# Kernel optimization log

Measured on AMD Instinct MI355X. Metric: run time of the kernel, lower is better.

The kernel has to match this reference:

```python
import jax, jax.numpy as jnp
import numpy as np

B, S, E, H, D = 384, 128, 512, 4, 128  # batch, seq(block), embed, heads, head_dim


def setup_inputs() -> dict:
    key = jax.random.key(0)
    ks = jax.random.split(key, 6)
    scale = 1.0 / np.sqrt(E)  # lecun_normal-ish fan-in scaling
    return {
        "x": jax.random.normal(ks[0], (B, S, E), dtype=jnp.float32),
        "Wq": jax.random.normal(ks[1], (E, E), dtype=jnp.float32) * scale,
        "bq": jnp.zeros((E,), dtype=jnp.float32),
        "Wk": jax.random.normal(ks[2], (E, E), dtype=jnp.float32) * scale,
        "bk": jnp.zeros((E,), dtype=jnp.float32),
        "Wv": jax.random.normal(ks[3], (E, E), dtype=jnp.float32) * scale,
        "bv": jnp.zeros((E,), dtype=jnp.float32),
        "Wo": jax.random.normal(ks[4], (E, E), dtype=jnp.float32) * scale,
        "bo": jnp.zeros((E,), dtype=jnp.float32),
    }


def reference(x, Wq, bq, Wk, bk, Wv, bv, Wo, bo):
    # Projections, then split heads: [B,S,E] -> [B,S,H,D]
    q = (x @ Wq + bq).reshape(B, S, H, D)
    k = (x @ Wk + bk).reshape(B, S, H, D)
    v = (x @ Wv + bv).reshape(B, S, H, D)
    # NOTE: original applies no 1/sqrt(D) scaling and no mask.
    scores = jnp.einsum("BSHD,BTHD->BHST", q, k)  # [B,H,S,T]
    weights = jax.nn.softmax(scores, axis=-1)
    out = jnp.einsum("BHST,BTHD->BSHD", weights, v).reshape(B, S, E)
    return out @ Wo + bo
```

## Files before the change

### kernel.cpp

```cpp
#include <hip/hip_runtime.h>
#include <hip/hip_bf16.h>
#include <cstdint>


#define EMB 512

typedef __attribute__((ext_vector_type(4))) float    f32x4;
typedef __attribute__((ext_vector_type(8))) _Float16 f16x8;

#define MFMA16(a, b, c) __builtin_amdgcn_mfma_f32_16x16x32_f16((a), (b), (c), 0, 0, 0)

__device__ __forceinline__ int swz128(int row, int col) {
    return row * 128 + (col ^ (((row >> 2) & 3) << 4));
}
__device__ __forceinline__ int swz64(int row, int col) {
    return row * 64 + (col ^ (((row >> 2) & 3) << 4));
}

__device__ __forceinline__ void gld_lds16(const _Float16* g, _Float16* l) {
    __builtin_amdgcn_global_load_lds(
        (const __attribute__((address_space(1))) void*)g,
        (__attribute__((address_space(3))) void*)l, 16, 0, 0);
}

__device__ __forceinline__ void stage64(_Float16* lds, const _Float16* gbase,
                                        int grow0, int k0, int wave, int lane) {
#pragma unroll
    for (int i = 0; i < 4; ++i) {
        int idx = wave * 256 + i * 64 + lane;
        int n   = idx >> 3;
        int kb  = (idx & 7) ^ (((n >> 2) & 3) << 1);
        gld_lds16(gbase + (grow0 + n) * EMB + k0 + kb * 8,
                  lds + wave * 2048 + i * 512);
    }
}

#define ZACC(A)                                   \
    _Pragma("unroll") for (int _i = 0; _i < 2; ++_i) \
    _Pragma("unroll") for (int _j = 0; _j < 8; ++_j) \
        A[_i][_j] = (f32x4){0.f, 0.f, 0.f, 0.f};

__global__ void k_prep(const float* __restrict__ x, _Float16* __restrict__ xh,
                       const float* __restrict__ Wq, const float* __restrict__ Wk,
                       const float* __restrict__ Wv, const float* __restrict__ Wo,
                       _Float16* __restrict__ Wqkvt, _Float16* __restrict__ Wot) {
    __shared__ float t[32][33];
    const int g = blockIdx.x, tid = threadIdx.x;
    if (g < 12288) {
        long i = ((long)g * 256 + tid) * 8;
        f32x4 a = *(const f32x4*)(x + i);
        f32x4 b = *(const f32x4*)(x + i + 4);
        f16x8 o;
        o[0] = (_Float16)a[0]; o[1] = (_Float16)a[1];
        o[2] = (_Float16)a[2]; o[3] = (_Float16)a[3];
        o[4] = (_Float16)b[0]; o[5] = (_Float16)b[1];
        o[6] = (_Float16)b[2]; o[7] = (_Float16)b[3];
        *(f16x8*)(xh + i) = o;
        return;
    }
    const int tb = g - 12288;
    const int z = tb >> 8, t2 = tb & 255;
    const float* W = (z == 0) ? Wq : (z == 1) ? Wk : (z == 2) ? Wv : Wo;
    _Float16* Wt = (z < 3) ? (Wqkvt + (long)z * 512 * EMB) : Wot;
    const int tx = tid & 31, ty = tid >> 5;
    const int k0 = (t2 & 15) * 32, n0 = (t2 >> 4) * 32;
#pragma unroll
    for (int i = 0; i < 4; ++i)
        t[ty + i * 8][tx] = W[(k0 + ty + i * 8) * EMB + n0 + tx];
    __syncthreads();
#pragma unroll
    for (int i = 0; i < 4; ++i)
        Wt[(n0 + ty + i * 8) * EMB + k0 + tx] = (_Float16)t[tx][ty + i * 8];
}

__global__ __launch_bounds__(256, 4)
void k_qkv(const _Float16* __restrict__ xh, const _Float16* __restrict__ Wqkvt,
           const float* __restrict__ bq, const float* __restrict__ bk,
           const float* __restrict__ bv,
           _Float16* __restrict__ qb, _Float16* __restrict__ kb,
           _Float16* __restrict__ vtb) {
    __shared__ _Float16 S[2][128 * 64];
    _Float16* SA = S[0];
    _Float16* SB = S[1];
    const int tid = threadIdx.x, wave = tid >> 6, lane = tid & 63;
    const int l15 = lane & 15, quad = lane >> 4;
    const int g = blockIdx.x;
    const int xcd = g & 7, r = g >> 3;
    const int bb = xcd * 48 + r / 12, j = r % 12;
    const int m0 = bb * 128;
    const bool vswap = (j >= 8);
    const _Float16* As = vswap ? SB : SA;
    const _Float16* Bs = vswap ? SA : SB;
    f32x4 acc[2][8];
    ZACC(acc);
    for (int k0 = 0; k0 < EMB; k0 += 64) {
        stage64(SA, xh, m0, k0, wave, lane);
        stage64(SB, Wqkvt, j * 128, k0, wave, lane);
        __syncthreads();
#pragma unroll
        for (int ktl = 0; ktl < 2; ++ktl) {
            int cb = ktl * 32 + quad * 8;
            f16x8 a0 = *(const f16x8*)&As[swz64(wave * 32 + l15, cb)];
            f16x8 a1 = *(const f16x8*)&As[swz64(wave * 32 + 16 + l15, cb)];
#pragma unroll
            for (int nt = 0; nt < 8; ++nt) {
                f16x8 bbf = *(const f16x8*)&Bs[swz64(nt * 16 + l15, cb)];
                acc[0][nt] = MFMA16(a0, bbf, acc[0][nt]);
                acc[1][nt] = MFMA16(a1, bbf, acc[1][nt]);
            }
        }
        __syncthreads();
    }
    _Float16* SC = &S[0][0];
    if (!vswap) {
        const float* bias = (j < 4) ? bq : bk;
        const int nc0 = (j & 3) * 128;
#pragma unroll
        for (int nt = 0; nt < 8; ++nt) {
            int col = nt * 16 + l15;
            float bz = bias[nc0 + col];
#pragma unroll
            for (int mt = 0; mt < 2; ++mt)
#pragma unroll
                for (int rr = 0; rr < 4; ++rr) {
                    int row = wave * 32 + mt * 16 + quad * 4 + rr;
                    SC[swz128(row, col)] = (_Float16)(acc[mt][nt][rr] + bz);
                }
        }
        __syncthreads();
        _Float16* dst = (j < 4) ? qb : kb;
#pragma unroll
        for (int i = 0; i < 8; ++i) {
            int idx = i * 256 + tid;
            int row = idx >> 4, col = (idx & 15) * 8;
            f16x8 v = *(const f16x8*)&SC[row * 128 + (col ^ (((row >> 2) & 3) << 4))];
            *(f16x8*)(dst + (long)(m0 + row) * EMB + nc0 + col) = v;
        }
    } else {
        const int hv = j - 8;
#pragma unroll
        for (int mt = 0; mt < 2; ++mt)
#pragma unroll
            for (int rr = 0; rr < 4; ++rr) {
                int row = wave * 32 + mt * 16 + quad * 4 + rr;
                float bz = bv[hv * 128 + row];
#pragma unroll
                for (int nt = 0; nt < 8; ++nt) {
                    int col = nt * 16 + l15;
                    SC[swz128(row, col)] = (_Float16)(acc[mt][nt][rr] + bz);
                }
            }
        __syncthreads();
        _Float16* dst = vtb + (long)(bb * 4 + hv) * 128 * 128;
#pragma unroll
        for (int i = 0; i < 8; ++i) {
            int idx = i * 256 + tid;
            int row = idx >> 4, col = (idx & 15) * 8;
            f16x8 v = *(const f16x8*)&SC[row * 128 + (col ^ (((row >> 2) & 3) << 4))];
            *(f16x8*)(dst + row * 128 + col) = v;
        }
    }
}

__global__ __launch_bounds__(256, 4)
void k_core(const _Float16* __restrict__ qb, const _Float16* __restrict__ kb,
            const _Float16* __restrict__ vtb, _Float16* __restrict__ attn) {
    __shared__ _Float16 SP[128 * 128];
    const int tid = threadIdx.x, wave = tid >> 6, lane = tid & 63;
    const int l15 = lane & 15, quad = lane >> 4;
    const int g = blockIdx.x;
    const int xcd = g & 7, r = g >> 3;
    const int b = xcd * 48 + (r >> 2), h = r & 3;
    const int sRow0 = b * 128, wRow0 = h * 128;
    const _Float16* vt = vtb + (long)(b * 4 + h) * 128 * 128;
    f32x4 acc[2][8];

    ZACC(acc);
#pragma unroll
    for (int kt = 0; kt < 4; ++kt) {
        int ca = kt * 32 + quad * 8;
        const _Float16* qrow = qb + (long)(sRow0 + wave * 32 + l15) * EMB + wRow0 + ca;
        f16x8 q0 = *(const f16x8*)qrow;
        f16x8 q1 = *(const f16x8*)(qrow + 16 * EMB);
#pragma unroll
        for (int nt = 0; nt < 8; ++nt) {
            f16x8 kf = *(const f16x8*)(kb + (long)(sRow0 + nt * 16 + l15) * EMB + wRow0 + ca);
            acc[0][nt] = MFMA16(q0, kf, acc[0][nt]);
            acc[1][nt] = MFMA16(q1, kf, acc[1][nt]);
        }
    }
#pragma unroll
    for (int mt = 0; mt < 2; ++mt)
#pragma unroll
        for (int rr = 0; rr < 4; ++rr) {
            float mx = acc[mt][0][rr];
#pragma unroll
            for (int nt = 1; nt < 8; ++nt) mx = fmaxf(mx, acc[mt][nt][rr]);
            mx = fmaxf(mx, __shfl_xor(mx, 1));
            mx = fmaxf(mx, __shfl_xor(mx, 2));
            mx = fmaxf(mx, __shfl_xor(mx, 4));
            mx = fmaxf(mx, __shfl_xor(mx, 8));
            float sm = 0.f;
#pragma unroll
            for (int nt = 0; nt < 8; ++nt) {
                float e = __expf(acc[mt][nt][rr] - mx);
                acc[mt][nt][rr] = e;
                sm += e;
            }
            sm += __shfl_xor(sm, 1);
            sm += __shfl_xor(sm, 2);
            sm += __shfl_xor(sm, 4);
            sm += __shfl_xor(sm, 8);
            float inv = 1.0f / sm;
#pragma unroll
            for (int nt = 0; nt < 8; ++nt) acc[mt][nt][rr] *= inv;
        }

#pragma unroll
    for (int mt = 0; mt < 2; ++mt)
#pragma unroll
        for (int nt = 0; nt < 8; ++nt) {
            int col = nt * 16 + l15;
#pragma unroll
            for (int rr = 0; rr < 4; ++rr) {
                int row = wave * 32 + mt * 16 + quad * 4 + rr;
                SP[swz128(row, col)] = (_Float16)acc[mt][nt][rr];
            }
        }
    __syncthreads();

    ZACC(acc);
#pragma unroll
    for (int kt = 0; kt < 4; ++kt) {
        int ca = kt * 32 + quad * 8;
        int rp = wave * 32 + l15;
        f16x8 p0 = *(const f16x8*)&SP[swz128(rp, ca)];
        f16x8 p1 = *(const f16x8*)&SP[swz128(rp + 16, ca)];
#pragma unroll
        for (int nt = 0; nt < 8; ++nt) {
            f16x8 vf = *(const f16x8*)(vt + (nt * 16 + l15) * 128 + ca);
            acc[0][nt] = MFMA16(p0, vf, acc[0][nt]);
            acc[1][nt] = MFMA16(p1, vf, acc[1][nt]);
        }
    }
    __syncthreads();

#pragma unroll
    for (int mt = 0; mt < 2; ++mt)
#pragma unroll
        for (int nt = 0; nt < 8; ++nt) {
            int col = nt * 16 + l15;
#pragma unroll
            for (int rr = 0; rr < 4; ++rr) {
                int row = wave * 32 + mt * 16 + quad * 4 + rr;
                SP[swz128(row, col)] = (_Float16)acc[mt][nt][rr];
            }
        }
    __syncthreads();
#pragma unroll
    for (int i = 0; i < 8; ++i) {
        int idx = i * 256 + tid;
        int row = idx >> 4, col = (idx & 15) * 8;
        f16x8 v = *(const f16x8*)&SP[row * 128 + (col ^ (((row >> 2) & 3) << 4))];
        *(f16x8*)(attn + (long)(sRow0 + row) * EMB + wRow0 + col) = v;
    }
}

__global__ __launch_bounds__(256, 4)
void k_out(const _Float16* __restrict__ attn, const _Float16* __restrict__ Wot,
           const float* __restrict__ bo, float* __restrict__ out) {
    __shared__ _Float16 SA[128 * 64];
    __shared__ _Float16 SB[128 * 64];
    const int tid = threadIdx.x, wave = tid >> 6, lane = tid & 63;
    const int l15 = lane & 15, quad = lane >> 4;
    const int g = blockIdx.x;
    const int xcd = g & 7, r = g >> 3;
    const int m0 = (xcd * 48 + (r >> 2)) * 128, n0 = (r & 3) * 128;
    f32x4 acc[2][8];
    ZACC(acc);
    for (int k0 = 0; k0 < EMB; k0 += 64) {
        stage64(SA, attn, m0, k0, wave, lane);
        stage64(SB, Wot, n0, k0, wave, lane);
        __syncthreads();
#pragma unroll
        for (int ktl = 0; ktl < 2; ++ktl) {
            int ra = wave * 32 + l15;
            int cb = ktl * 32 + quad * 8;
            f16x8 a0 = *(const f16x8*)&SA[swz64(ra, cb)];
            f16x8 a1 = *(const f16x8*)&SA[swz64(ra + 16, cb)];
#pragma unroll
            for (int nt = 0; nt < 8; ++nt) {
                f16x8 bb = *(const f16x8*)&SB[swz64(nt * 16 + l15, cb)];
                acc[0][nt] = MFMA16(a0, bb, acc[0][nt]);
                acc[1][nt] = MFMA16(a1, bb, acc[1][nt]);
            }
        }
        __syncthreads();
    }
#pragma unroll
    for (int nt = 0; nt < 8; ++nt) {
        int col = n0 + nt * 16 + l15;
        float bias = bo[col];
#pragma unroll
        for (int mt = 0; mt < 2; ++mt)
#pragma unroll
            for (int rr = 0; rr < 4; ++rr) {
                int row = m0 + wave * 32 + mt * 16 + quad * 4 + rr;
                out[(long)row * EMB + col] = acc[mt][nt][rr] + bias;
            }
    }
}

extern "C" void kernel_launch(void* const* d_in, const int* in_sizes, int n_in,
                              void* d_out, int out_size, void* d_ws, size_t ws_size,
                              hipStream_t stream) {
    const float* x  = (const float*)d_in[0];
    const float* Wq = (const float*)d_in[1];
    const float* bq = (const float*)d_in[2];
    const float* Wk = (const float*)d_in[3];
    const float* bk = (const float*)d_in[4];
    const float* Wv = (const float*)d_in[5];
    const float* bv = (const float*)d_in[6];
    const float* Wo = (const float*)d_in[7];
    const float* bo = (const float*)d_in[8];
    float* out = (float*)d_out;

    char* w = (char*)d_ws;
    _Float16* xh    = (_Float16*)(w);
    _Float16* attn  = xh;
    _Float16* Wqkvt = (_Float16*)(w + 50331648);
    _Float16* Wot   = (_Float16*)(w + 51904512);
    _Float16* qb    = (_Float16*)(w + 52428800);
    _Float16* kb    = (_Float16*)(w + 102760448);
    _Float16* vtb   = (_Float16*)(w + 153092096);

    k_prep<<<13312, 256, 0, stream>>>(x, xh, Wq, Wk, Wv, Wo, Wqkvt, Wot);
    k_qkv<<<4608, 256, 0, stream>>>(xh, Wqkvt, bq, bk, bv, qb, kb, vtb);
    k_core<<<1536, 256, 0, stream>>>(qb, kb, vtb, attn);
    k_out<<<1536, 256, 0, stream>>>(attn, Wot, bo, out);
}
```

Measured before the change: 378.7 us.

## Stage K/V in LDS for attention core and retile output projection

k_core now runs 512 threads (8 waves, 16 query rows each) and loads K and V^T into swizzled LDS with global_load_lds, instead of each wave reading K/V straight from global memory. k_out is retiled to 64-row tiles with twice as many blocks, stages its operands with direct-to-LDS loads, and writes output through an LDS transpose as coalesced float4 stores. The aim is to cut redundant global traffic, raise parallelism, and make the output stores coalesced. In exchange, LDS use and thread count per block go up, which may lower occupancy, and the smaller k_out tile reuses each Wo tile across fewer rows.

Result: faster. 370.1 us (-2.3%).

```diff
diff --git a/kernel.cpp b/kernel.cpp
--- a/kernel.cpp
+++ b/kernel.cpp
@@ -162,10 +162,11 @@
     }
 }
 
-__global__ __launch_bounds__(256, 4)
+__global__ __launch_bounds__(512, 4)
 void k_core(const _Float16* __restrict__ qb, const _Float16* __restrict__ kb,
             const _Float16* __restrict__ vtb, _Float16* __restrict__ attn) {
-    __shared__ _Float16 SP[128 * 128];
+    __shared__ _Float16 SK[128 * 128];
+    __shared__ _Float16 SV[128 * 128];
     const int tid = threadIdx.x, wave = tid >> 6, lane = tid & 63;
     const int l15 = lane & 15, quad = lane >> 4;
     const int g = blockIdx.x;
@@ -173,95 +174,94 @@
     const int b = xcd * 48 + (r >> 2), h = r & 3;
     const int sRow0 = b * 128, wRow0 = h * 128;
     const _Float16* vt = vtb + (long)(b * 4 + h) * 128 * 128;
-    f32x4 acc[2][8];
-
-    ZACC(acc);
+
+#pragma unroll
+    for (int i = 0; i < 4; ++i) {
+        int seg = i * 8 + wave;
+        int idx = seg * 64 + lane;
+        int n   = idx >> 4;
+        int kbk = (idx & 15) ^ (((n >> 2) & 3) << 1);
+        gld_lds16(kb + (long)(sRow0 + n) * EMB + wRow0 + kbk * 8, SK + seg * 512);
+        gld_lds16(vt + n * 128 + kbk * 8, SV + seg * 512);
+    }
+    __syncthreads();
+
+    f32x4 acc[8];
+#pragma unroll
+    for (int nt = 0; nt < 8; ++nt) acc[nt] = (f32x4){0.f, 0.f, 0.f, 0.f};
+
 #pragma unroll
     for (int kt = 0; kt < 4; ++kt) {
         int ca = kt * 32 + quad * 8;
-        const _Float16* qrow = qb + (long)(sRow0 + wave * 32 + l15) * EMB + wRow0 + ca;
-        f16x8 q0 = *(const f16x8*)qrow;
-        f16x8 q1 = *(const f16x8*)(qrow + 16 * EMB);
+        f16x8 q0 = *(const f16x8*)(qb + (long)(sRow0 + wave * 16 + l15) * EMB + wRow0 + ca);
 #pragma unroll
         for (int nt = 0; nt < 8; ++nt) {
-            f16x8 kf = *(const f16x8*)(kb + (long)(sRow0 + nt * 16 + l15) * EMB + wRow0 + ca);
-            acc[0][nt] = MFMA16(q0, kf, acc[0][nt]);
-            acc[1][nt] = MFMA16(q1, kf, acc[1][nt]);
-        }
-    }
-#pragma unroll
-    for (int mt = 0; mt < 2; ++mt)
-#pragma unroll
-        for (int rr = 0; rr < 4; ++rr) {
-            float mx = acc[mt][0][rr];
-#pragma unroll
-            for (int nt = 1; nt < 8; ++nt) mx = fmaxf(mx, acc[mt][nt][rr]);
-            mx = fmaxf(mx, __shfl_xor(mx, 1));
-            mx = fmaxf(mx, __shfl_xor(mx, 2));
-            mx = fmaxf(mx, __shfl_xor(mx, 4));
-            mx = fmaxf(mx, __shfl_xor(mx, 8));
-            float sm = 0.f;
-#pragma unroll
-            for (int nt = 0; nt < 8; ++nt) {
-                float e = __expf(acc[mt][nt][rr] - mx);
-                acc[mt][nt][rr] = e;
-                sm += e;
-            }
-            sm += __shfl_xor(sm, 1);
-            sm += __shfl_xor(sm, 2);
-            sm += __shfl_xor(sm, 4);
-            sm += __shfl_xor(sm, 8);
-            float inv = 1.0f / sm;
-#pragma unroll
-            for (int nt = 0; nt < 8; ++nt) acc[mt][nt][rr] *= inv;
-        }
-
-#pragma unroll
-    for (int mt = 0; mt < 2; ++mt)
+            f16x8 kf = *(const f16x8*)&SK[swz128(nt * 16 + l15, ca)];
+            acc[nt] = MFMA16(q0, kf, acc[nt]);
+        }
+    }
+#pragma unroll
+    for (int rr = 0; rr < 4; ++rr) {
+        float mx = acc[0][rr];
+#pragma unroll
+        for (int nt = 1; nt < 8; ++nt) mx = fmaxf(mx, acc[nt][rr]);
+        mx = fmaxf(mx, __shfl_xor(mx, 1));
+        mx = fmaxf(mx, __shfl_xor(mx, 2));
+        mx = fmaxf(mx, __shfl_xor(mx, 4));
+        mx = fmaxf(mx, __shfl_xor(mx, 8));
+        float sm = 0.f;
 #pragma unroll
         for (int nt = 0; nt < 8; ++nt) {
-            int col = nt * 16 + l15;
-#pragma unroll
-            for (int rr = 0; rr < 4; ++rr) {
-                int row = wave * 32 + mt * 16 + quad * 4 + rr;
-                SP[swz128(row, col)] = (_Float16)acc[mt][nt][rr];
-            }
-        }
-    __syncthreads();
-
-    ZACC(acc);
+            float e = __expf(acc[nt][rr] - mx);
+            acc[nt][rr] = e;
+            sm += e;
+        }
+        sm += __shfl_xor(sm, 1);
+        sm += __shfl_xor(sm, 2);
+        sm += __shfl_xor(sm, 4);
+        sm += __shfl_xor(sm, 8);
+        float inv = 1.0f / sm;
+#pragma unroll
+        for (int nt = 0; nt < 8; ++nt) acc[nt][rr] *= inv;
+    }
+    __syncthreads();
+
+#pragma unroll
+    for (int nt = 0; nt < 8; ++nt) {
+        int col = nt * 16 + l15;
+#pragma unroll
+        for (int rr = 0; rr < 4; ++rr)
+            SK[swz128(wave * 16 + quad * 4 + rr, col)] = (_Float16)acc[nt][rr];
+    }
+    __syncthreads();
+
+#pragma unroll
+    for (int nt = 0; nt < 8; ++nt) acc[nt] = (f32x4){0.f, 0.f, 0.f, 0.f};
 #pragma unroll
     for (int kt = 0; kt < 4; ++kt) {
         int ca = kt * 32 + quad * 8;
-        int rp = wave * 32 + l15;
-        f16x8 p0 = *(const f16x8*)&SP[swz128(rp, ca)];
-        f16x8 p1 = *(const f16x8*)&SP[swz128(rp + 16, ca)];
+        f16x8 p0 = *(const f16x8*)&SK[swz128(wave * 16 + l15, ca)];
 #pragma unroll
         for (int nt = 0; nt < 8; ++nt) {
-            f16x8 vf = *(const f16x8*)(vt + (nt * 16 + l15) * 128 + ca);
-            acc[0][nt] = MFMA16(p0, vf, acc[0][nt]);
-            acc[1][nt] = MFMA16(p1, vf, acc[1][nt]);
-        }
-    }
-    __syncthreads();
-
-#pragma unroll
-    for (int mt = 0; mt < 2; ++mt)
-#pragma unroll
-        for (int nt = 0; nt < 8; ++nt) {
-            int col = nt * 16 + l15;
-#pragma unroll
-            for (int rr = 0; rr < 4; ++rr) {
-                int row = wave * 32 + mt * 16 + quad * 4 + rr;
-                SP[swz128(row, col)] = (_Float16)acc[mt][nt][rr];
-            }
-        }
-    __syncthreads();
-#pragma unroll
-    for (int i = 0; i < 8; ++i) {
-        int idx = i * 256 + tid;
+            f16x8 vf = *(const f16x8*)&SV[swz128(nt * 16 + l15, ca)];
+            acc[nt] = MFMA16(p0, vf, acc[nt]);
+        }
+    }
+    __syncthreads();
+
+#pragma unroll
+    for (int nt = 0; nt < 8; ++nt) {
+        int col = nt * 16 + l15;
+#pragma unroll
+        for (int rr = 0; rr < 4; ++rr)
+            SV[swz128(wave * 16 + quad * 4 + rr, col)] = (_Float16)acc[nt][rr];
+    }
+    __syncthreads();
+#pragma unroll
+    for (int i = 0; i < 4; ++i) {
+        int idx = i * 512 + tid;
         int row = idx >> 4, col = (idx & 15) * 8;
-        f16x8 v = *(const f16x8*)&SP[row * 128 + (col ^ (((row >> 2) & 3) << 4))];
+        f16x8 v = *(const f16x8*)&SV[row * 128 + (col ^ (((row >> 2) & 3) << 4))];
         *(f16x8*)(attn + (long)(sRow0 + row) * EMB + wRow0 + col) = v;
     }
 }
@@ -269,45 +269,63 @@
 __global__ __launch_bounds__(256, 4)
 void k_out(const _Float16* __restrict__ attn, const _Float16* __restrict__ Wot,
            const float* __restrict__ bo, float* __restrict__ out) {
-    __shared__ _Float16 SA[128 * 64];
-    __shared__ _Float16 SB[128 * 64];
+    __shared__ _Float16 SH[16384];
+    _Float16* SA = SH;
+    _Float16* SB = SH + 4096;
     const int tid = threadIdx.x, wave = tid >> 6, lane = tid & 63;
     const int l15 = lane & 15, quad = lane >> 4;
     const int g = blockIdx.x;
     const int xcd = g & 7, r = g >> 3;
-    const int m0 = (xcd * 48 + (r >> 2)) * 128, n0 = (r & 3) * 128;
-    f32x4 acc[2][8];
-    ZACC(acc);
+    const int m0 = (xcd * 96 + (r >> 2)) * 64, n0 = (r & 3) * 128;
+    f32x4 acc[8];
+#pragma unroll
+    for (int nt = 0; nt < 8; ++nt) acc[nt] = (f32x4){0.f, 0.f, 0.f, 0.f};
     for (int k0 = 0; k0 < EMB; k0 += 64) {
-        stage64(SA, attn, m0, k0, wave, lane);
-        stage64(SB, Wot, n0, k0, wave, lane);
+#pragma unroll
+        for (int i = 0; i < 2; ++i) {
+            int seg = i * 4 + wave;
+            int idx = seg * 64 + lane;
+            int n = idx >> 3, kbk = (idx & 7) ^ (((n >> 2) & 3) << 1);
+            gld_lds16(attn + (long)(m0 + n) * EMB + k0 + kbk * 8, SA + seg * 512);
+        }
+#pragma unroll
+        for (int i = 0; i < 4; ++i) {
+            int seg = i * 4 + wave;
+            int idx = seg * 64 + lane;
+            int n = idx >> 3, kbk = (idx & 7) ^ (((n >> 2) & 3) << 1);
+            gld_lds16(Wot + (long)(n0 + n) * EMB + k0 + kbk * 8, SB + seg * 512);
+        }
         __syncthreads();
 #pragma unroll
         for (int ktl = 0; ktl < 2; ++ktl) {
-            int ra = wave * 32 + l15;
             int cb = ktl * 32 + quad * 8;
-            f16x8 a0 = *(const f16x8*)&SA[swz64(ra, cb)];
-            f16x8 a1 = *(const f16x8*)&SA[swz64(ra + 16, cb)];
+            f16x8 a0 = *(const f16x8*)&SA[swz64(wave * 16 + l15, cb)];
 #pragma unroll
             for (int nt = 0; nt < 8; ++nt) {
                 f16x8 bb = *(const f16x8*)&SB[swz64(nt * 16 + l15, cb)];
-                acc[0][nt] = MFMA16(a0, bb, acc[0][nt]);
-                acc[1][nt] = MFMA16(a1, bb, acc[1][nt]);
+                acc[nt] = MFMA16(a0, bb, acc[nt]);
             }
         }
         __syncthreads();
     }
+    float* SF = (float*)SH;
 #pragma unroll
     for (int nt = 0; nt < 8; ++nt) {
-        int col = n0 + nt * 16 + l15;
-        float bias = bo[col];
-#pragma unroll
-        for (int mt = 0; mt < 2; ++mt)
-#pragma unroll
-            for (int rr = 0; rr < 4; ++rr) {
-                int row = m0 + wave * 32 + mt * 16 + quad * 4 + rr;
-                out[(long)row * EMB + col] = acc[mt][nt][rr] + bias;
-            }
+        int col = nt * 16 + l15;
+        float bz = bo[n0 + col];
+#pragma unroll
+        for (int rr = 0; rr < 4; ++rr) {
+            int row = wave * 16 + quad * 4 + rr;
+            SF[row * 128 + (col ^ (((row >> 2) & 1) << 4))] = acc[nt][rr] + bz;
+        }
+    }
+    __syncthreads();
+#pragma unroll
+    for (int i = 0; i < 8; ++i) {
+        int idx = i * 256 + tid;
+        int row = idx >> 5, c4 = (idx & 31) * 4;
+        f32x4 v = *(const f32x4*)&SF[row * 128 + (c4 ^ (((row >> 2) & 1) << 4))];
+        *(f32x4*)(out + (long)(m0 + row) * EMB + n0 + c4) = v;
     }
 }
 
@@ -336,6 +354,6 @@
 
     k_prep<<<13312, 256, 0, stream>>>(x, xh, Wq, Wk, Wv, Wo, Wqkvt, Wot);
     k_qkv<<<4608, 256, 0, stream>>>(xh, Wqkvt, bq, bk, bv, qb, kb, vtb);
-    k_core<<<1536, 256, 0, stream>>>(qb, kb, vtb, attn);
-    k_out<<<1536, 256, 0, stream>>>(attn, Wot, bo, out);
-}
+    k_core<<<1536, 512, 0, stream>>>(qb, kb, vtb, attn);
+    k_out<<<3072, 256, 0, stream>>>(attn, Wot, bo, out);
+}
```
